# Performance work log

Hardware: AMD Instinct MI355X
Metric: run time of the kernel (lower is better)

Reference implementation:

```python
import jax, jax.numpy as jnp
import numpy as np

B = 8192          # number of jagged segments
SUF = 256         # suffix length appended per segment


def setup_inputs() -> dict:
    key = jax.random.key(0)
    k1, k2 = jax.random.split(key)
    rng = np.random.RandomState(0)
    lengths = rng.randint(1024, 3072, size=B).astype(np.int64)  # mean ~2048
    prefix_sum = np.cumsum(lengths)                              # inclusive prefix sum
    n_vals = int(prefix_sum[-1])
    values = jax.random.normal(k1, (n_vals,), dtype=jnp.float32)
    suffix_mat = jax.random.normal(k2, (B, SUF), dtype=jnp.float32)
    return {
        "values": values,
        "prefix_sum": jnp.asarray(prefix_sum, dtype=jnp.int64),
        "suffix_mat": suffix_mat,
    }


def reference(values, prefix_sum, suffix_mat):
    # Jagged append: out = concat_i( values[seg_i] ++ suffix_mat[i] )
    b, suf = suffix_mat.shape
    n_vals = values.shape[0]
    n_out = n_vals + b * suf
    # inclusive prefix sum of output segment lengths (each old len + suf)
    new_prefix = prefix_sum + (jnp.arange(1, b + 1, dtype=prefix_sum.dtype)) * suf
    j = jnp.arange(n_out, dtype=prefix_sum.dtype)
    # segment id for each output position
    seg = jnp.searchsorted(new_prefix, j, side="right")
    prev_old = jnp.where(seg > 0, prefix_sum[jnp.maximum(seg - 1, 0)], 0)  # old start offset
    new_start = prev_old + seg * suf                                        # new start offset
    local = j - new_start                                                   # pos within out segment
    seg_len = prefix_sum[seg] - prev_old                                    # old segment length
    in_vals = local < seg_len
    val_idx = jnp.clip(prev_old + local, 0, n_vals - 1)
    suf_idx = jnp.clip(local - seg_len, 0, suf - 1)
    return jnp.where(in_vals, values[val_idx], suffix_mat[seg, suf_idx])
```

## Files before the change

kernel.cpp:

```cpp
#include <hip/hip_runtime.h>


#define SUF 256
#define NTHR 256
#define TILE 1024

typedef float floatx4 __attribute__((ext_vector_type(4)));

__global__ __launch_bounds__(NTHR) void
jagged_append_tiled(const float* __restrict__ values,
                    const int* __restrict__ prefix_sum,
                    const float* __restrict__ suffix,
                    float* __restrict__ out,
                    int B) {
    const int seg = blockIdx.x >> 2;
    const int t   = blockIdx.x & 3;
    const int tid = threadIdx.x;
    if (seg >= B) return;

    const int prev_old = (seg > 0) ? prefix_sum[seg - 1] : 0;
    const int end_old  = prefix_sum[seg];
    const int seg_len  = end_old - prev_old;
    const int new_start = prev_old + seg * SUF;

    if (t == 3) {
        const float* __restrict__ sfx = suffix + seg * SUF;
        float* __restrict__ sdst = out + new_start + seg_len;
        sdst[tid] = sfx[tid];
        return;
    }

    const int t0 = t * TILE;
    int t1 = t0 + TILE;
    if (t1 > seg_len) t1 = seg_len;
    if (t0 >= t1) return;
    const int n = t1 - t0;

    const float* __restrict__ src = values + prev_old + t0;
    float* __restrict__ dst = out + new_start + t0;

    int head = (4 - (((unsigned)(size_t)dst >> 2) & 3)) & 3;
    if (head > n) head = n;
    if (tid < head) dst[tid] = src[tid];

    const int nvec = (n - head) >> 2;
    if (tid < nvec) {
        const floatx4* __restrict__ vs = (const floatx4*)(src + head);
        floatx4* __restrict__ vd = (floatx4*)(dst + head);
        vd[tid] = vs[tid];
    }

    const int tail = head + (nvec << 2);
    if (tid < n - tail) dst[tail + tid] = src[tail + tid];
}

extern "C" void kernel_launch(void* const* d_in, const int* in_sizes, int n_in,
                              void* d_out, int out_size, void* d_ws, size_t ws_size,
                              hipStream_t stream) {
    const float* values     = (const float*)d_in[0];
    const int*   prefix_sum = (const int*)d_in[1];
    const float* suffix     = (const float*)d_in[2];
    float* out = (float*)d_out;

    const int B = in_sizes[1];

    jagged_append_tiled<<<4 * B, NTHR, 0, stream>>>(values, prefix_sum, suffix,
                                                    out, B);
}
```

Before: 35.83 us.

## Process two whole segments per block with strided loops instead of four tile blocks

Replaces the four-blocks-per-segment grid (three value tiles plus one suffix block) with one block handling two consecutive segments. Each block loops over the whole segment with strided float4 copies and also copies the suffix with vectorized unaligned-source loads. This cuts block count and launch/scheduling overhead, and reuses the shared prefix_sum load between the two segments. In exchange it serializes more work per block, lowering parallelism and adding per-segment load imbalance.

```diff
diff --git a/kernel.cpp b/kernel.cpp
--- a/kernel.cpp
+++ b/kernel.cpp
@@ -3,55 +3,64 @@
 
 #define SUF 256
 #define NTHR 256
-#define TILE 1024
 
 typedef float floatx4 __attribute__((ext_vector_type(4)));
 
-__global__ __launch_bounds__(NTHR) void
-jagged_append_tiled(const float* __restrict__ values,
-                    const int* __restrict__ prefix_sum,
-                    const float* __restrict__ suffix,
-                    float* __restrict__ out,
-                    int B) {
-    const int seg = blockIdx.x >> 2;
-    const int t   = blockIdx.x & 3;
-    const int tid = threadIdx.x;
-    if (seg >= B) return;
-
-    const int prev_old = (seg > 0) ? prefix_sum[seg - 1] : 0;
-    const int end_old  = prefix_sum[seg];
-    const int seg_len  = end_old - prev_old;
-    const int new_start = prev_old + seg * SUF;
-
-    if (t == 3) {
-        const float* __restrict__ sfx = suffix + seg * SUF;
-        float* __restrict__ sdst = out + new_start + seg_len;
-        sdst[tid] = sfx[tid];
-        return;
-    }
-
-    const int t0 = t * TILE;
-    int t1 = t0 + TILE;
-    if (t1 > seg_len) t1 = seg_len;
-    if (t0 >= t1) return;
-    const int n = t1 - t0;
-
-    const float* __restrict__ src = values + prev_old + t0;
-    float* __restrict__ dst = out + new_start + t0;
-
+__device__ __forceinline__ void copy_same_phase(const float* __restrict__ src,
+                                                float* __restrict__ dst,
+                                                int n, int tid) {
     int head = (4 - (((unsigned)(size_t)dst >> 2) & 3)) & 3;
     if (head > n) head = n;
     if (tid < head) dst[tid] = src[tid];
+    const int nvec = (n - head) >> 2;
+    const floatx4* __restrict__ vs = (const floatx4*)(src + head);
+    floatx4* __restrict__ vd = (floatx4*)(dst + head);
+    for (int v = tid; v < nvec; v += NTHR) vd[v] = vs[v];
+    for (int i = head + (nvec << 2) + tid; i < n; i += NTHR) dst[i] = src[i];
+}
 
-    const int nvec = (n - head) >> 2;
+__device__ __forceinline__ void copy_suffix(const float* __restrict__ sfx,
+                                            float* __restrict__ dst, int tid) {
+    const int head = (4 - (((unsigned)(size_t)dst >> 2) & 3)) & 3;
+    if (tid < head) dst[tid] = sfx[tid];
+    const int nvec = (SUF - head) >> 2;
     if (tid < nvec) {
-        const floatx4* __restrict__ vs = (const floatx4*)(src + head);
-        floatx4* __restrict__ vd = (floatx4*)(dst + head);
-        vd[tid] = vs[tid];
+        floatx4 v;
+        __builtin_memcpy(&v, sfx + head + tid * 4, 16);
+        *(floatx4*)(dst + head + tid * 4) = v;
+    }
+    const int tail = head + (nvec << 2);
+    if (tid < SUF - tail) dst[tail + tid] = sfx[tail + tid];
+}
+
+__global__ __launch_bounds__(NTHR) void
+jagged_append_kernel(const float* __restrict__ values,
+                     const int* __restrict__ prefix_sum,
+                     const float* __restrict__ suffix,
+                     float* __restrict__ out,
+                     int B) {
+    const int tid = threadIdx.x;
+    const int seg0 = blockIdx.x * 2;
+    if (seg0 >= B) return;
+
+    const int ps_m1 = (seg0 > 0) ? prefix_sum[seg0 - 1] : 0;
+    const int ps0   = prefix_sum[seg0];
+
+    {
+        const int seg_len = ps0 - ps_m1;
+        float* __restrict__ dst = out + ps_m1 + seg0 * SUF;
+        copy_same_phase(values + ps_m1, dst, seg_len, tid);
+        copy_suffix(suffix + seg0 * SUF, dst + seg_len, tid);
     }
 
-    const int tail = head + (nvec << 2);
-    if (tid < n - tail) dst[tail + tid] = src[tail + tid];
+    const int seg1 = seg0 + 1;
+    if (seg1 < B) {
+        const int ps1 = prefix_sum[seg1];
+        const int seg_len = ps1 - ps0;
+        float* __restrict__ dst = out + ps0 + seg1 * SUF;
+        copy_same_phase(values + ps0, dst, seg_len, tid);
+        copy_suffix(suffix + seg1 * SUF, dst + seg_len, tid);
+    }
 }
 
 extern "C" void kernel_launch(void* const* d_in, const int* in_sizes, int n_in,
@@ -63,7 +72,8 @@
     float* out = (float*)d_out;
 
     const int B = in_sizes[1];
+    const int nblocks = (B + 1) / 2;
 
-    jagged_append_tiled<<<4 * B, NTHR, 0, stream>>>(values, prefix_sum, suffix,
-                                                    out, B);
+    jagged_append_kernel<<<nblocks, NTHR, 0, stream>>>(values, prefix_sum,
+                                                       suffix, out, B);
 }
```

After: 30.24 us. 1.18x faster.
